# Kernel tuning notes

Measured on AMD Instinct MI355X. Metric: run time of the kernel, lower is better.

The kernel has to match this reference:

```python
import jax, jax.numpy as jnp
import numpy as np

B, H, S, D = 2, 12, 2048, 64

def setup_inputs() -> dict:
    key = jax.random.key(0)
    kq, kk, kv = jax.random.split(key, 3)
    query = jax.random.normal(kq, (B, H, S, D), dtype=jnp.float32)
    k = jax.random.normal(kk, (B, H, S, D), dtype=jnp.float32)
    value = jax.random.normal(kv, (B, H, S, D), dtype=jnp.float32)
    # causal mask: 1 where allowed, 0 where masked
    mask = jnp.tril(jnp.ones((S, S), dtype=jnp.int32))[None, None, :, :]
    return {"query": query, "key": k, "value": value, "mask": mask}

def reference(query, key, value, mask):
    # qk: [B,H,S,S]
    qk = jnp.einsum('bhqd,bhkd->bhqk', query, key) / jnp.sqrt(jnp.float32(key.shape[-1]))
    # faithful quirk of the source: masked positions set to 1e-9 (not -inf)
    qk = jnp.where(mask == 0, jnp.float32(1e-9), qk)
    attention_weights = jax.nn.softmax(qk, axis=-1)
    out = jnp.einsum('bhqk,bhkd->bhqd', attention_weights, value)
    # note: self.dropout is defined but never applied in the original forward
    return out, attention_weights
```

## Files before the change

kernel.cpp:

```cpp
#include <hip/hip_runtime.h>

typedef unsigned short ushort_t;
typedef __attribute__((ext_vector_type(8))) short bf16x8;
typedef __attribute__((ext_vector_type(4))) float f32x4;

__device__ __forceinline__ unsigned short f2bf(float x) {
  union { float f; unsigned u; } v; v.f = x;
  unsigned r = v.u + 0x7fffu + ((v.u >> 16) & 1u);
  return (unsigned short)(r >> 16);
}

namespace {

constexpr int S  = 2048;
constexpr int D  = 64;
constexpr int BH = 24;
constexpr float SHIFT = 5.0f;

__global__ __launch_bounds__(256)
void cvtQK(const float* __restrict__ Q, const float* __restrict__ K,
           ushort_t* __restrict__ Qb, ushort_t* __restrict__ Kb) {
  const int b = blockIdx.x;
  const bool isK = (b >= 1536);
  const float* src = isK ? K : Q;
  ushort_t* dst = isK ? Kb : Qb;
  const size_t i = (size_t)(isK ? b - 1536 : b) * 256 + threadIdx.x;
  const float4* s4 = (const float4*)src;
  const float4 a = s4[2 * i], c = s4[2 * i + 1];
  const float x[8] = {a.x, a.y, a.z, a.w, c.x, c.y, c.z, c.w};
  bf16x8 h;
#pragma unroll
  for (int j = 0; j < 8; ++j) h[j] = (short)f2bf(x[j]);
  *(bf16x8*)(dst + 8 * i) = h;
}

__global__ __launch_bounds__(256)
void vt16c(const float* __restrict__ V, ushort_t* __restrict__ vt,
           float* __restrict__ pref) {
  const int bh = blockIdx.y, kc = blockIdx.x, t = threadIdx.x;
  __shared__ float tile[64][65];
  const float* vp = V + ((size_t)(bh * S + kc * 64)) * D;
#pragma unroll
  for (int i = 0; i < 4; ++i) {
    const int e4 = i * 256 + t;
    const int row = e4 >> 4, c4 = (e4 & 15) * 4;
    const float4 v = *(const float4*)(vp + row * 64 + c4);
    tile[row][c4 + 0] = v.x; tile[row][c4 + 1] = v.y;
    tile[row][c4 + 2] = v.z; tile[row][c4 + 3] = v.w;
  }
  __syncthreads();
  if (t < 64) {
    float s = 0.f;
#pragma unroll 8
    for (int j = 0; j < 64; ++j) s += tile[j][t];
    pref[((size_t)bh * 33 + kc) * 64 + t] = s;
  }
#pragma unroll
  for (int i = 0; i < 2; ++i) {
    const int e8 = i * 256 + t;
    const int d = e8 >> 3, k8 = (e8 & 7) * 8;
    bf16x8 h;
#pragma unroll
    for (int j = 0; j < 8; ++j) h[j] = (short)f2bf(tile[k8 + j][d]);
    *(bf16x8*)(vt + ((size_t)(bh * 64 + d)) * S + kc * 64 + k8) = h;
  }
}

__global__ __launch_bounds__(64)
void scan_pref(float* __restrict__ pref) {
  const int bh = blockIdx.x, d = threadIdx.x;
  float run = 0.f;
  for (int kc = 0; kc < 32; ++kc) {
    float* p = pref + ((size_t)bh * 33 + kc) * 64 + d;
    const float t = *p; *p = run; run += t;
  }
  pref[((size_t)bh * 33 + 32) * 64 + d] = run;
}

__global__ __launch_bounds__(128)
void attn4(const ushort_t* __restrict__ Qb, const ushort_t* __restrict__ Kb,
           const ushort_t* __restrict__ VTb, const float* __restrict__ pref,
           float* __restrict__ out, float* __restrict__ wts) {
  const int id  = blockIdx.x;
  const int xcd = id & 7;
  const int j   = id >> 3;
  const int grp = j >> 5;
  const int bh  = xcd * 3 + grp;
  const int pp  = ((j & 31) * 11 + grp * 7) & 31;

  const int tid = threadIdx.x;
  const int wv  = tid >> 6;
  const int l   = tid & 63;
  const int l15 = l & 15;
  const int g   = l >> 4;

  __shared__ __align__(16) ushort_t kbuf[2][64 * 64];
  __shared__ __align__(16) ushort_t vbuf[2][64 * 64];

  const ushort_t* Kbh = Kb  + (size_t)bh * S * D;
  const ushort_t* Vbh = VTb + (size_t)bh * D * S;
  const float cMask = __expf(1e-9f - SHIFT);

  auto stageK = [&](int buf, int kc) {
#pragma unroll
    for (int i = 0; i < 4; ++i) {
      const int gran = i * 128 + tid;
      const int row = gran >> 3, slot = gran & 7;
      const ushort_t* gp = Kbh + (size_t)(kc * 64 + row) * D + ((slot ^ (row & 7)) * 8);
      ushort_t* lp = kbuf[buf] + (size_t)(i * 128 + wv * 64) * 8;
      __builtin_amdgcn_global_load_lds((const __attribute__((address_space(1))) void*)gp,
                                       (__attribute__((address_space(3))) void*)lp, 16, 0, 0);
    }
  };
  auto stageV = [&](int buf, int kc) {
#pragma unroll
    for (int i = 0; i < 4; ++i) {
      const int gran = i * 128 + tid;
      const int row = gran >> 3, slot = gran & 7;
      const ushort_t* gp = Vbh + (size_t)row * S + kc * 64 + ((slot ^ (row & 7)) * 8);
      ushort_t* lp = vbuf[buf] + (size_t)(i * 128 + wv * 64) * 8;
      __builtin_amdgcn_global_load_lds((const __attribute__((address_space(1))) void*)gp,
                                       (__attribute__((address_space(3))) void*)lp, 16, 0, 0);
    }
  };

  for (int ti = 0; ti < 2; ++ti) {
    const int t   = ti ? (63 - pp) : pp;
    const int qw  = t * 32 + wv * 16;
    const int nch = (t >> 1) + 1;
    const int q   = qw + l15;

    bf16x8 qh[2];
    {
      const size_t qo = ((size_t)(bh * S + q)) * D + g * 8;
      qh[0] = *(const bf16x8*)(Qb + qo);
      qh[1] = *(const bf16x8*)(Qb + qo + 32);
    }

    auto qk = [&](int buf, int kc, f32x4* sacc) {
#pragma unroll
      for (int kt = 0; kt < 4; ++kt) {
        sacc[kt] = f32x4{0.f, 0.f, 0.f, 0.f};
        if (kc * 64 + kt * 16 <= qw + 15) {
#pragma unroll
          for (int ks = 0; ks < 2; ++ks) {
            const int row = kt * 16 + l15;
            const bf16x8 kf = *(const bf16x8*)(kbuf[buf] + row * 64 + (((ks * 4 + g) ^ (row & 7)) * 8));
            sacc[kt] = __builtin_amdgcn_mfma_f32_16x16x32_bf16(kf, qh[ks], sacc[kt], 0, 0, 0);
          }
        }
      }
    };

    float Zp = 0.f;
    stageK(0, 0);
    __syncthreads();
    for (int kc = 0; kc < nch; ++kc) {
      const int cur = kc & 1;
      if (kc + 1 < nch) stageK(cur ^ 1, kc + 1);
      f32x4 sacc[4];
      qk(cur, kc, sacc);
#pragma unroll
      for (int kt = 0; kt < 4; ++kt) {
        if (kc * 64 + kt * 16 <= qw + 15) {
          const int kbase = kc * 64 + kt * 16 + 4 * g;
#pragma unroll
          for (int r = 0; r < 4; ++r) {
            const float s = (kbase + r <= q) ? sacc[kt][r] * 0.125f : 1e-9f;
            Zp += __expf(s - SHIFT);
          }
        } else {
          Zp += 4.f * cMask;
        }
      }
      __syncthreads();
    }
    Zp += __shfl_xor(Zp, 16);
    Zp += __shfl_xor(Zp, 32);
    const float Z     = Zp + (float)(S - nch * 64) * cMask;
    const float invZ  = 1.f / Z;
    const float wmask = cMask * invZ;

    f32x4 oacc[4];
#pragma unroll
    for (int dt = 0; dt < 4; ++dt) oacc[dt] = f32x4{0.f, 0.f, 0.f, 0.f};

    stageK(0, 0); stageV(0, 0);
    __syncthreads();
    for (int kc = 0; kc < nch; ++kc) {
      const int cur = kc & 1;
      if (kc + 1 < nch) { stageK(cur ^ 1, kc + 1); stageV(cur ^ 1, kc + 1); }
      f32x4 sacc[4];
      qk(cur, kc, sacc);

      int pk[4][2];
#pragma unroll
      for (int kt = 0; kt < 4; ++kt) {
        const int kbase = kc * 64 + kt * 16 + 4 * g;
        f32x4 w4;
        if (kc * 64 + kt * 16 <= qw + 15) {
#pragma unroll
          for (int r = 0; r < 4; ++r) {
            const float s = (kbase + r <= q) ? sacc[kt][r] * 0.125f : 1e-9f;
            w4[r] = __expf(s - SHIFT) * invZ;
          }
        } else {
          w4 = f32x4{wmask, wmask, wmask, wmask};
        }
        __builtin_nontemporal_store(w4, (f32x4*)&wts[((size_t)(bh * S + q)) * S + kbase]);
        asm("v_cvt_pk_bf16_f32 %0, %1, %2" : "=v"(pk[kt][0]) : "v"(w4[0]), "v"(w4[1]));
        asm("v_cvt_pk_bf16_f32 %0, %1, %2" : "=v"(pk[kt][1]) : "v"(w4[2]), "v"(w4[3]));
      }

      const int srcA = l15 + ((g & 1) * 2) * 16;
      const int srcB = srcA + 16;
      const bool hi = (g & 2) != 0;
#pragma unroll
      for (int ks = 0; ks < 2; ++ks) {
        const int a0 = __shfl(pk[ks * 2][0], srcA);
        const int a1 = __shfl(pk[ks * 2][1], srcA);
        const int a2 = __shfl(pk[ks * 2][0], srcB);
        const int a3 = __shfl(pk[ks * 2][1], srcB);
        const int b0 = __shfl(pk[ks * 2 + 1][0], srcA);
        const int b1 = __shfl(pk[ks * 2 + 1][1], srcA);
        const int b2 = __shfl(pk[ks * 2 + 1][0], srcB);
        const int b3 = __shfl(pk[ks * 2 + 1][1], srcB);
        union { int d[4]; bf16x8 v; } u;
        u.d[0] = hi ? b0 : a0;
        u.d[1] = hi ? b1 : a1;
        u.d[2] = hi ? b2 : a2;
        u.d[3] = hi ? b3 : a3;
        const bf16x8 pa = u.v;
#pragma unroll
        for (int dt = 0; dt < 4; ++dt) {
          const int row = dt * 16 + l15;
          const bf16x8 vf = *(const bf16x8*)(vbuf[cur] + row * 64 + (((ks * 4 + g) ^ (row & 7)) * 8));
          oacc[dt] = __builtin_amdgcn_mfma_f32_16x16x32_bf16(pa, vf, oacc[dt], 0, 0, 0);
        }
      }
      __syncthreads();
    }

    float wm[4];
#pragma unroll
    for (int r = 0; r < 4; ++r) wm[r] = __shfl(wmask, 4 * g + r);
    const float* prefBH = pref + (size_t)bh * 33 * 64;
#pragma unroll
    for (int dt = 0; dt < 4; ++dt) {
      const int d = dt * 16 + l15;
      const float suf = prefBH[32 * 64 + d] - prefBH[nch * 64 + d];
#pragma unroll
      for (int r = 0; r < 4; ++r) {
        out[((size_t)(bh * S + qw + 4 * g + r)) * D + d] = oacc[dt][r] + wm[r] * suf;
      }
    }
    const int fillStart = nch * 64;
#pragma unroll
    for (int r16 = 0; r16 < 16; ++r16) {
      const float w = __shfl(wmask, r16);
      const f32x4 w4 = {w, w, w, w};
      float* rowp = wts + ((size_t)(bh * S + qw + r16)) * S;
      for (int c = fillStart + l * 4; c < S; c += 256) {
        __builtin_nontemporal_store(w4, (f32x4*)(rowp + c));
      }
    }
  }
}

}

extern "C" void kernel_launch(void* const* d_in, const int* in_sizes, int n_in,
                              void* d_out, int out_size, void* d_ws, size_t ws_size,
                              hipStream_t stream) {
  const float* Q = (const float*)d_in[0];
  const float* K = (const float*)d_in[1];
  const float* V = (const float*)d_in[2];
  float* out = (float*)d_out;
  float* wts = out + (size_t)BH * S * D;

  char* ws = (char*)d_ws;
  const size_t T = (size_t)BH * S * D * 2;
  ushort_t* Qb   = (ushort_t*)(ws + 0 * T);
  ushort_t* Kb   = (ushort_t*)(ws + 1 * T);
  ushort_t* VTb  = (ushort_t*)(ws + 2 * T);
  float*    pref = (float*)(ws + 3 * T);

  cvtQK<<<3072, 256, 0, stream>>>(Q, K, Qb, Kb);
  vt16c<<<dim3(32, BH), 256, 0, stream>>>(V, VTb, pref);
  scan_pref<<<BH, 64, 0, stream>>>(pref);
  attn4<<<768, 128, 0, stream>>>(Qb, Kb, VTb, pref, out, wts);
}
```

Measured before the change: 141.6 us.

## Process paired causal tiles concurrently with 4 waves sharing K/V staging

Replaces the sequential two-tile loop (each block handling tile pp and then 63-pp with 2 waves) with a 256-thread block where waves 0-1 take the long tile and waves 2-3 the short tile at the same time. K/V chunks staged in shared memory are reused by both tiles, so the short tile's chunk loads are no longer issued a second time, and the block has more waves in flight to hide latency. The short-tile waves sit idle at barriers while the long tile finishes its extra chunks. The pp permutation is also dropped, which changes how tiles map to blocks.

```diff
diff --git a/kernel.cpp b/kernel.cpp
--- a/kernel.cpp
+++ b/kernel.cpp
@@ -77,8 +77,8 @@
   pref[((size_t)bh * 33 + 32) * 64 + d] = run;
 }
 
-__global__ __launch_bounds__(128)
-void attn4(const ushort_t* __restrict__ Qb, const ushort_t* __restrict__ Kb,
+__global__ __launch_bounds__(256)
+void attn6(const ushort_t* __restrict__ Qb, const ushort_t* __restrict__ Kb,
            const ushort_t* __restrict__ VTb, const float* __restrict__ pref,
            float* __restrict__ out, float* __restrict__ wts) {
   const int id  = blockIdx.x;
@@ -86,7 +86,7 @@
   const int j   = id >> 3;
   const int grp = j >> 5;
   const int bh  = xcd * 3 + grp;
-  const int pp  = ((j & 31) * 11 + grp * 7) & 31;
+  const int pp  = j & 31;
 
   const int tid = threadIdx.x;
   const int wv  = tid >> 6;
@@ -94,6 +94,12 @@
   const int l15 = l & 15;
   const int g   = l >> 4;
 
+  const int tw    = (wv < 2) ? (63 - pp) : pp;
+  const int qw    = tw * 32 + (wv & 1) * 16;
+  const int nch_w = (tw >> 1) + 1;
+  const int nmax  = ((63 - pp) >> 1) + 1;
+  const int q     = qw + l15;
+
   __shared__ __align__(16) ushort_t kbuf[2][64 * 64];
   __shared__ __align__(16) ushort_t vbuf[2][64 * 64];
 
@@ -103,61 +109,56 @@
 
   auto stageK = [&](int buf, int kc) {
 #pragma unroll
-    for (int i = 0; i < 4; ++i) {
-      const int gran = i * 128 + tid;
+    for (int i = 0; i < 2; ++i) {
+      const int gran = i * 256 + tid;
       const int row = gran >> 3, slot = gran & 7;
       const ushort_t* gp = Kbh + (size_t)(kc * 64 + row) * D + ((slot ^ (row & 7)) * 8);
-      ushort_t* lp = kbuf[buf] + (size_t)(i * 128 + wv * 64) * 8;
+      ushort_t* lp = kbuf[buf] + (size_t)(i * 256 + wv * 64) * 8;
       __builtin_amdgcn_global_load_lds((const __attribute__((address_space(1))) void*)gp,
                                        (__attribute__((address_space(3))) void*)lp, 16, 0, 0);
     }
   };
   auto stageV = [&](int buf, int kc) {
 #pragma unroll
-    for (int i = 0; i < 4; ++i) {
-      const int gran = i * 128 + tid;
+    for (int i = 0; i < 2; ++i) {
+      const int gran = i * 256 + tid;
       const int row = gran >> 3, slot = gran & 7;
       const ushort_t* gp = Vbh + (size_t)row * S + kc * 64 + ((slot ^ (row & 7)) * 8);
-      ushort_t* lp = vbuf[buf] + (size_t)(i * 128 + wv * 64) * 8;
+      ushort_t* lp = vbuf[buf] + (size_t)(i * 256 + wv * 64) * 8;
       __builtin_amdgcn_global_load_lds((const __attribute__((address_space(1))) void*)gp,
                                        (__attribute__((address_space(3))) void*)lp, 16, 0, 0);
     }
   };
 
-  for (int ti = 0; ti < 2; ++ti) {
-    const int t   = ti ? (63 - pp) : pp;
-    const int qw  = t * 32 + wv * 16;
-    const int nch = (t >> 1) + 1;
-    const int q   = qw + l15;
-
-    bf16x8 qh[2];
-    {
-      const size_t qo = ((size_t)(bh * S + q)) * D + g * 8;
-      qh[0] = *(const bf16x8*)(Qb + qo);
-      qh[1] = *(const bf16x8*)(Qb + qo + 32);
-    }
-
-    auto qk = [&](int buf, int kc, f32x4* sacc) {
-#pragma unroll
-      for (int kt = 0; kt < 4; ++kt) {
-        sacc[kt] = f32x4{0.f, 0.f, 0.f, 0.f};
-        if (kc * 64 + kt * 16 <= qw + 15) {
-#pragma unroll
-          for (int ks = 0; ks < 2; ++ks) {
-            const int row = kt * 16 + l15;
-            const bf16x8 kf = *(const bf16x8*)(kbuf[buf] + row * 64 + (((ks * 4 + g) ^ (row & 7)) * 8));
-            sacc[kt] = __builtin_amdgcn_mfma_f32_16x16x32_bf16(kf, qh[ks], sacc[kt], 0, 0, 0);
-          }
-        }
-      }
-    };
-
-    float Zp = 0.f;
-    stageK(0, 0);
-    __syncthreads();
-    for (int kc = 0; kc < nch; ++kc) {
-      const int cur = kc & 1;
-      if (kc + 1 < nch) stageK(cur ^ 1, kc + 1);
+  bf16x8 qh[2];
+  {
+    const size_t qo = ((size_t)(bh * S + q)) * D + g * 8;
+    qh[0] = *(const bf16x8*)(Qb + qo);
+    qh[1] = *(const bf16x8*)(Qb + qo + 32);
+  }
+
+  auto qk = [&](int buf, int kc, f32x4* sacc) {
+#pragma unroll
+    for (int kt = 0; kt < 4; ++kt) {
+      sacc[kt] = f32x4{0.f, 0.f, 0.f, 0.f};
+      if (kc * 64 + kt * 16 <= qw + 15) {
+#pragma unroll
+        for (int ks = 0; ks < 2; ++ks) {
+          const int row = kt * 16 + l15;
+          const bf16x8 kf = *(const bf16x8*)(kbuf[buf] + row * 64 + (((ks * 4 + g) ^ (row & 7)) * 8));
+          sacc[kt] = __builtin_amdgcn_mfma_f32_16x16x32_bf16(kf, qh[ks], sacc[kt], 0, 0, 0);
+        }
+      }
+    }
+  };
+
+  float Zp = 0.f;
+  stageK(0, 0);
+  __syncthreads();
+  for (int kc = 0; kc < nmax; ++kc) {
+    const int cur = kc & 1;
+    if (kc + 1 < nmax) stageK(cur ^ 1, kc + 1);
+    if (kc < nch_w) {
       f32x4 sacc[4];
       qk(cur, kc, sacc);
 #pragma unroll
@@ -173,23 +174,25 @@
           Zp += 4.f * cMask;
         }
       }
-      __syncthreads();
-    }
-    Zp += __shfl_xor(Zp, 16);
-    Zp += __shfl_xor(Zp, 32);
-    const float Z     = Zp + (float)(S - nch * 64) * cMask;
-    const float invZ  = 1.f / Z;
-    const float wmask = cMask * invZ;
-
-    f32x4 oacc[4];
-#pragma unroll
-    for (int dt = 0; dt < 4; ++dt) oacc[dt] = f32x4{0.f, 0.f, 0.f, 0.f};
-
-    stageK(0, 0); stageV(0, 0);
+    }
     __syncthreads();
-    for (int kc = 0; kc < nch; ++kc) {
-      const int cur = kc & 1;
-      if (kc + 1 < nch) { stageK(cur ^ 1, kc + 1); stageV(cur ^ 1, kc + 1); }
+  }
+  Zp += __shfl_xor(Zp, 16);
+  Zp += __shfl_xor(Zp, 32);
+  const float Z     = Zp + (float)(S - nch_w * 64) * cMask;
+  const float invZ  = 1.f / Z;
+  const float wmask = cMask * invZ;
+
+  f32x4 oacc[4];
+#pragma unroll
+  for (int dt = 0; dt < 4; ++dt) oacc[dt] = f32x4{0.f, 0.f, 0.f, 0.f};
+
+  stageK(0, 0); stageV(0, 0);
+  __syncthreads();
+  for (int kc = 0; kc < nmax; ++kc) {
+    const int cur = kc & 1;
+    if (kc + 1 < nmax) { stageK(cur ^ 1, kc + 1); stageV(cur ^ 1, kc + 1); }
+    if (kc < nch_w) {
       f32x4 sacc[4];
       qk(cur, kc, sacc);
 
@@ -238,31 +241,31 @@
           oacc[dt] = __builtin_amdgcn_mfma_f32_16x16x32_bf16(pa, vf, oacc[dt], 0, 0, 0);
         }
       }
-      __syncthreads();
-    }
-
-    float wm[4];
-#pragma unroll
-    for (int r = 0; r < 4; ++r) wm[r] = __shfl(wmask, 4 * g + r);
-    const float* prefBH = pref + (size_t)bh * 33 * 64;
-#pragma unroll
-    for (int dt = 0; dt < 4; ++dt) {
-      const int d = dt * 16 + l15;
-      const float suf = prefBH[32 * 64 + d] - prefBH[nch * 64 + d];
-#pragma unroll
-      for (int r = 0; r < 4; ++r) {
-        out[((size_t)(bh * S + qw + 4 * g + r)) * D + d] = oacc[dt][r] + wm[r] * suf;
-      }
-    }
-    const int fillStart = nch * 64;
-#pragma unroll
-    for (int r16 = 0; r16 < 16; ++r16) {
-      const float w = __shfl(wmask, r16);
-      const f32x4 w4 = {w, w, w, w};
-      float* rowp = wts + ((size_t)(bh * S + qw + r16)) * S;
-      for (int c = fillStart + l * 4; c < S; c += 256) {
-        __builtin_nontemporal_store(w4, (f32x4*)(rowp + c));
-      }
+    }
+    __syncthreads();
+  }
+
+  float wm[4];
+#pragma unroll
+  for (int r = 0; r < 4; ++r) wm[r] = __shfl(wmask, 4 * g + r);
+  const float* prefBH = pref + (size_t)bh * 33 * 64;
+#pragma unroll
+  for (int dt = 0; dt < 4; ++dt) {
+    const int d = dt * 16 + l15;
+    const float suf = prefBH[32 * 64 + d] - prefBH[nch_w * 64 + d];
+#pragma unroll
+    for (int r = 0; r < 4; ++r) {
+      out[((size_t)(bh * S + qw + 4 * g + r)) * D + d] = oacc[dt][r] + wm[r] * suf;
+    }
+  }
+  const int fillStart = nch_w * 64;
+#pragma unroll
+  for (int r16 = 0; r16 < 16; ++r16) {
+    const float w = __shfl(wmask, r16);
+    const f32x4 w4 = {w, w, w, w};
+    float* rowp = wts + ((size_t)(bh * S + qw + r16)) * S;
+    for (int c = fillStart + l * 4; c < S; c += 256) {
+      __builtin_nontemporal_store(w4, (f32x4*)(rowp + c));
     }
   }
 }
@@ -288,5 +291,5 @@
   cvtQK<<<3072, 256, 0, stream>>>(Q, K, Qb, Kb);
   vt16c<<<dim3(32, BH), 256, 0, stream>>>(V, VTb, pref);
   scan_pref<<<BH, 64, 0, stream>>>(pref);
-  attn4<<<768, 128, 0, stream>>>(Qb, Kb, VTb, pref, out, wts);
-}
+  attn6<<<768, 256, 0, stream>>>(Qb, Kb, VTb, pref, out, wts);
+}
```

Result: slower. 173.4 us (+22.4%).
